# Kernel optimization log

Hardware: AMD Instinct MI355X
Metric: run time of the kernel (lower is better)

## Reference

```python
import jax, jax.numpy as jnp
import numpy as np

B, N, L = 64, 256, 1024
OUT = L // 2   # ChebConv out_channels = Seq_len / 2
ALPHA = 0.5    # DirGNNConv default alpha


def _glorot(key, shape):
    # PyG ChebConv lins use glorot init
    lim = float(np.sqrt(6.0 / (shape[0] + shape[1])))
    return jax.random.uniform(key, shape, minval=-lim, maxval=lim, dtype=jnp.float32)


def setup_inputs() -> dict:
    key = jax.random.key(0)
    ks = jax.random.split(key, 8)
    x = jax.random.normal(ks[0], (B, N, L), dtype=jnp.float32)
    # dense per-sample adjacency; only used via nonzero() in torch, never enters math (K=1)
    At = jax.random.randint(ks[1], (B, N, N), 0, 2, dtype=jnp.int32)
    W_in = _glorot(ks[2], (L, OUT))
    b_in = jnp.zeros((OUT,), dtype=jnp.float32)
    W_out = _glorot(ks[3], (L, OUT))
    b_out = jnp.zeros((OUT,), dtype=jnp.float32)
    # DirGNNConv root Linear (kaiming-ish uniform; exact init irrelevant for correctness baseline)
    lim = float(1.0 / np.sqrt(L))
    W_root = jax.random.uniform(ks[4], (L, OUT), minval=-lim, maxval=lim, dtype=jnp.float32)
    b_root = jax.random.uniform(ks[5], (OUT,), minval=-lim, maxval=lim, dtype=jnp.float32)
    return {"x": x, "At": At, "W_in": W_in, "b_in": b_in,
            "W_out": W_out, "b_out": b_out, "W_root": W_root, "b_root": b_root}


def reference(x, At, W_in, b_in, W_out, b_out, W_root, b_root):
    # so the batched edge_index built from At.nonzero() never influences the output.
    # DirGNNConv: alpha * conv_out(x) + (1-alpha) * conv_in(x) + root_lin(x).
    xf = x.reshape(B * N, L)                        # [B*N, L]
    y = (ALPHA * (xf @ W_out + b_out)
         + (1.0 - ALPHA) * (xf @ W_in + b_in)
         + (xf @ W_root + b_root))                  # [B*N, OUT]
    return y.reshape(B, N, OUT)
```

## Files before the change

kernel.cpp:

```cpp
#include <hip/hip_runtime.h>
#include <stdint.h>

static constexpr int Kdim  = 1024;
static constexpr int Ncols = 512;

typedef __attribute__((ext_vector_type(8))) short bf16x8;
typedef __attribute__((ext_vector_type(4))) float f32x4;

__device__ __forceinline__ unsigned short f2bf(float f) {
  unsigned u = __builtin_bit_cast(unsigned, f);
  u += 0x7FFFu + ((u >> 16) & 1u);
  return (unsigned short)(u >> 16);
}
__device__ __forceinline__ unsigned f2bf2(float lo, float hi) {
  unsigned ul = __builtin_bit_cast(unsigned, lo);
  unsigned uh = __builtin_bit_cast(unsigned, hi);
  ul += 0x7FFFu + ((ul >> 16) & 1u);
  uh += 0x7FFFu + ((uh >> 16) & 1u);
  return (ul >> 16) | (uh & 0xFFFF0000u);
}

__device__ __forceinline__ void gl2lds16(const void* g, void* l) {
  __builtin_amdgcn_global_load_lds(
      (const __attribute__((address_space(1))) void*)g,
      (__attribute__((address_space(3))) void*)l, 16, 0, 0);
}

__global__ __launch_bounds__(256) void combine_w(
    const float* __restrict__ Win, const float* __restrict__ Wout,
    const float* __restrict__ Wroot, unsigned short* __restrict__ Wt)
{
  __shared__ unsigned short lds[32 * 36];
  const int bid = blockIdx.x;
  const int tk0 = (bid & 31) * 32;
  const int tn0 = (bid >> 5) * 32;
  const int t = threadIdx.x;
  {
    const int k  = t >> 3;
    const int nq = (t & 7) * 4;
    const int gi = (tk0 + k) * Ncols + tn0 + nq;
    const float4 wi = *(const float4*)(Win + gi);
    const float4 wo = *(const float4*)(Wout + gi);
    const float4 wr = *(const float4*)(Wroot + gi);
    lds[(nq + 0) * 36 + k] = f2bf(0.5f * (wi.x + wo.x) + wr.x);
    lds[(nq + 1) * 36 + k] = f2bf(0.5f * (wi.y + wo.y) + wr.y);
    lds[(nq + 2) * 36 + k] = f2bf(0.5f * (wi.z + wo.z) + wr.z);
    lds[(nq + 3) * 36 + k] = f2bf(0.5f * (wi.w + wo.w) + wr.w);
  }
  __syncthreads();
  {
    const int n  = t >> 3;
    const int k8 = (t & 7) * 4;
    const ushort4 v = *(const ushort4*)&lds[n * 36 + k8];
    *(ushort4*)(Wt + (size_t)(tn0 + n) * Kdim + tk0 + k8) = v;
  }
}

__global__ __launch_bounds__(256, 2) void gemm_fused2(
    const float* __restrict__ X, const unsigned short* __restrict__ Wt,
    const float* __restrict__ b_in, const float* __restrict__ b_out,
    const float* __restrict__ b_root, float* __restrict__ Y)
{
  __shared__ __attribute__((aligned(16))) short As[2 * 4096];
  __shared__ __attribute__((aligned(16))) short Bs[2 * 4096];

  const int bid = blockIdx.x;
  const int m0 = (bid & 127) * 128;
  const int n0 = (bid >> 7) * 128;

  const int t    = threadIdx.x;
  const int lane = t & 63;
  const int w    = t >> 6;
  const int wm   = w >> 1;
  const int wn   = w & 1;
  const int quad = lane >> 4;
  const int lm   = lane & 15;

  const int sr = t >> 1;
  const int sh = t & 1;
  const float* xp = X + (size_t)(m0 + sr) * Kdim + sh * 16;
  const int sw  = (sr >> 1) & 3;
  const int aw0 = sr * 32 + (((2 * sh) ^ sw) * 8);
  const int aw1 = sr * 32 + (((2 * sh + 1) ^ sw) * 8);

  const int srb = lane >> 2;
  const int ss  = lane & 3;
  const int sc  = ss ^ ((srb >> 1) & 3);
  const unsigned short* gB = Wt + (size_t)(n0 + w * 32 + srb) * Kdim + sc * 8;
  const int rowK = 16 * Kdim;
  const int lb0 = w * 1024;
  const int lb1 = w * 1024 + 512;

  const int slot = quad ^ ((lm >> 1) & 3);
  const int aoff = (wm * 64 + lm) * 32 + slot * 8;
  const int boff = (wn * 64 + lm) * 32 + slot * 8;

  f32x4 acc[4][4] = {};

  gl2lds16(gB,        &Bs[lb0]);
  gl2lds16(gB + rowK, &Bs[lb1]);
  {
    const float4 a0 = *(const float4*)(xp + 0);
    const float4 a1 = *(const float4*)(xp + 4);
    const float4 a2 = *(const float4*)(xp + 8);
    const float4 a3 = *(const float4*)(xp + 12);
    uint4 p0, p1;
    p0.x = f2bf2(a0.x, a0.y); p0.y = f2bf2(a0.z, a0.w);
    p0.z = f2bf2(a1.x, a1.y); p0.w = f2bf2(a1.z, a1.w);
    p1.x = f2bf2(a2.x, a2.y); p1.y = f2bf2(a2.z, a2.w);
    p1.z = f2bf2(a3.x, a3.y); p1.w = f2bf2(a3.z, a3.w);
    *(uint4*)&As[aw0] = p0;
    *(uint4*)&As[aw1] = p1;
  }

  #pragma unroll 1
  for (int it = 0; it < 32; ++it) {
    const int p = (it & 1) * 4096;
    const int q = p ^ 4096;
    __syncthreads();

    const int nx = (it < 31 ? it + 1 : 31) * 32;
    gl2lds16(gB + nx,        &Bs[q + lb0]);
    gl2lds16(gB + nx + rowK, &Bs[q + lb1]);
    const float4 a0 = *(const float4*)(xp + nx + 0);
    const float4 a1 = *(const float4*)(xp + nx + 4);
    const float4 a2 = *(const float4*)(xp + nx + 8);
    const float4 a3 = *(const float4*)(xp + nx + 12);

    bf16x8 af[4], bfr[4];
    #pragma unroll
    for (int i = 0; i < 4; ++i) af[i]  = *(const bf16x8*)&As[p + aoff + i * 512];
    #pragma unroll
    for (int j = 0; j < 4; ++j) bfr[j] = *(const bf16x8*)&Bs[p + boff + j * 512];
    #pragma unroll
    for (int i = 0; i < 4; ++i)
      #pragma unroll
      for (int j = 0; j < 4; ++j)
        acc[i][j] = __builtin_amdgcn_mfma_f32_16x16x32_bf16(af[i], bfr[j], acc[i][j], 0, 0, 0);

    uint4 p0, p1;
    p0.x = f2bf2(a0.x, a0.y); p0.y = f2bf2(a0.z, a0.w);
    p0.z = f2bf2(a1.x, a1.y); p0.w = f2bf2(a1.z, a1.w);
    p1.x = f2bf2(a2.x, a2.y); p1.y = f2bf2(a2.z, a2.w);
    p1.z = f2bf2(a3.x, a3.y); p1.w = f2bf2(a3.z, a3.w);
    *(uint4*)&As[q + aw0] = p0;
    *(uint4*)&As[q + aw1] = p1;
  }

  #pragma unroll
  for (int j = 0; j < 4; ++j) {
    const int gc = n0 + wn * 64 + j * 16 + lm;
    const float bias = 0.5f * (b_in[gc] + b_out[gc]) + b_root[gc];
    #pragma unroll
    for (int i = 0; i < 4; ++i) {
      const int gr = m0 + wm * 64 + i * 16 + quad * 4;
      float* yp = Y + (size_t)gr * Ncols + gc;
      #pragma unroll
      for (int r = 0; r < 4; ++r)
        yp[(size_t)r * Ncols] = acc[i][j][r] + bias;
    }
  }
}

extern "C" void kernel_launch(void* const* d_in, const int* in_sizes, int n_in,
                              void* d_out, int out_size, void* d_ws, size_t ws_size,
                              hipStream_t stream)
{
  const float* x      = (const float*)d_in[0];
  const float* W_in   = (const float*)d_in[2];
  const float* b_in   = (const float*)d_in[3];
  const float* W_out  = (const float*)d_in[4];
  const float* b_out  = (const float*)d_in[5];
  const float* W_root = (const float*)d_in[6];
  const float* b_root = (const float*)d_in[7];
  float* y = (float*)d_out;

  unsigned short* Wt = (unsigned short*)d_ws;

  combine_w <<<dim3(512), dim3(256), 0, stream>>>(W_in, W_out, W_root, Wt);
  gemm_fused2<<<dim3(512), dim3(256), 0, stream>>>(x, Wt, b_in, b_out, b_root, y);
}
```

Baseline: 161.4 us.

## Load fp32 X tiles directly to LDS and convert to bf16 at fragment read

The GEMM now streams the fp32 activation tile into LDS with asynchronous global_load_lds instead of loading into registers, converting, and storing bf16. The bf16 conversion moves to the point where each MFMA fragment is read from LDS. The M tile shrinks from 128 to 64 rows, which doubles the grid to 1024 blocks and raises the occupancy hint to 4 blocks per CU. B uses a new XOR swizzle. The aim is to take the global-load latency and conversion off the critical path and raise concurrency. The costs are more LDS traffic for fp32 A, repeated conversion work per wave, and less reuse of B per block.

```diff
diff --git a/kernel.cpp b/kernel.cpp
--- a/kernel.cpp
+++ b/kernel.cpp
@@ -6,6 +6,8 @@
 
 typedef __attribute__((ext_vector_type(8))) short bf16x8;
 typedef __attribute__((ext_vector_type(4))) float f32x4;
+
+union pk8 { uint4 u; bf16x8 h; };
 
 __device__ __forceinline__ unsigned short f2bf(float f) {
   unsigned u = __builtin_bit_cast(unsigned, f);
@@ -56,17 +58,17 @@
   }
 }
 
-__global__ __launch_bounds__(256, 2) void gemm_fused2(
+__global__ __launch_bounds__(256, 4) void gemm_fused3(
     const float* __restrict__ X, const unsigned short* __restrict__ Wt,
     const float* __restrict__ b_in, const float* __restrict__ b_out,
     const float* __restrict__ b_root, float* __restrict__ Y)
 {
-  __shared__ __attribute__((aligned(16))) short As[2 * 4096];
-  __shared__ __attribute__((aligned(16))) short Bs[2 * 4096];
+  __shared__ __attribute__((aligned(16))) float As[2][64 * 32];
+  __shared__ __attribute__((aligned(16))) short Bs[2][128 * 32];
 
   const int bid = blockIdx.x;
-  const int m0 = (bid & 127) * 128;
-  const int n0 = (bid >> 7) * 128;
+  const int m0 = (bid & 255) * 64;
+  const int n0 = (bid >> 8) * 128;
 
   const int t    = threadIdx.x;
   const int lane = t & 63;
@@ -76,75 +78,70 @@
   const int quad = lane >> 4;
   const int lm   = lane & 15;
 
-  const int sr = t >> 1;
-  const int sh = t & 1;
-  const float* xp = X + (size_t)(m0 + sr) * Kdim + sh * 16;
-  const int sw  = (sr >> 1) & 3;
-  const int aw0 = sr * 32 + (((2 * sh) ^ sw) * 8);
-  const int aw1 = sr * 32 + (((2 * sh + 1) ^ sw) * 8);
+  const int ra = lane >> 3;
+  const int sa = lane & 7;
+  const int ca = sa ^ ra;
+  const float* gA0 = X + (size_t)(m0 + w * 16 + ra) * Kdim + ca * 4;
+  const float* gA1 = gA0 + (size_t)8 * Kdim;
+  const int lA0 = (w * 16) * 32;
+  const int lA1 = (w * 16 + 8) * 32;
 
-  const int srb = lane >> 2;
-  const int ss  = lane & 3;
-  const int sc  = ss ^ ((srb >> 1) & 3);
-  const unsigned short* gB = Wt + (size_t)(n0 + w * 32 + srb) * Kdim + sc * 8;
-  const int rowK = 16 * Kdim;
-  const int lb0 = w * 1024;
-  const int lb1 = w * 1024 + 512;
+  const int rb = lane >> 2;
+  const int sb = lane & 3;
+  const int cb = sb ^ ((rb ^ (rb >> 2)) & 3);
+  const unsigned short* gB0 = Wt + (size_t)(n0 + w * 32 + rb) * Kdim + cb * 8;
+  const unsigned short* gB1 = gB0 + (size_t)16 * Kdim;
+  const int lB0 = (w * 32) * 32;
+  const int lB1 = (w * 32 + 16) * 32;
 
-  const int slot = quad ^ ((lm >> 1) & 3);
-  const int aoff = (wm * 64 + lm) * 32 + slot * 8;
-  const int boff = (wn * 64 + lm) * 32 + slot * 8;
+  const int sA0 = (2 * quad) ^ (lm & 7);
+  const int sA1 = sA0 ^ 1;
+  const int aoff = (wm * 32 + lm) * 32;
+  const int swzB = quad ^ ((lm ^ (lm >> 2)) & 3);
+  const int boff = (wn * 64 + lm) * 32 + swzB * 8;
 
-  f32x4 acc[4][4] = {};
+  f32x4 acc[2][4] = {};
 
-  gl2lds16(gB,        &Bs[lb0]);
-  gl2lds16(gB + rowK, &Bs[lb1]);
-  {
-    const float4 a0 = *(const float4*)(xp + 0);
-    const float4 a1 = *(const float4*)(xp + 4);
-    const float4 a2 = *(const float4*)(xp + 8);
-    const float4 a3 = *(const float4*)(xp + 12);
-    uint4 p0, p1;
-    p0.x = f2bf2(a0.x, a0.y); p0.y = f2bf2(a0.z, a0.w);
-    p0.z = f2bf2(a1.x, a1.y); p0.w = f2bf2(a1.z, a1.w);
-    p1.x = f2bf2(a2.x, a2.y); p1.y = f2bf2(a2.z, a2.w);
-    p1.z = f2bf2(a3.x, a3.y); p1.w = f2bf2(a3.z, a3.w);
-    *(uint4*)&As[aw0] = p0;
-    *(uint4*)&As[aw1] = p1;
-  }
+  gl2lds16(gA0, &As[0][lA0]);
+  gl2lds16(gA1, &As[0][lA1]);
+  gl2lds16(gB0, &Bs[0][lB0]);
+  gl2lds16(gB1, &Bs[0][lB1]);
 
   #pragma unroll 1
   for (int it = 0; it < 32; ++it) {
-    const int p = (it & 1) * 4096;
-    const int q = p ^ 4096;
+    const int p = it & 1;
+    const int q = p ^ 1;
     __syncthreads();
 
     const int nx = (it < 31 ? it + 1 : 31) * 32;
-    gl2lds16(gB + nx,        &Bs[q + lb0]);
-    gl2lds16(gB + nx + rowK, &Bs[q + lb1]);
-    const float4 a0 = *(const float4*)(xp + nx + 0);
-    const float4 a1 = *(const float4*)(xp + nx + 4);
-    const float4 a2 = *(const float4*)(xp + nx + 8);
-    const float4 a3 = *(const float4*)(xp + nx + 12);
+    gl2lds16(gA0 + nx, &As[q][lA0]);
+    gl2lds16(gA1 + nx, &As[q][lA1]);
+    gl2lds16(gB0 + nx, &Bs[q][lB0]);
+    gl2lds16(gB1 + nx, &Bs[q][lB1]);
 
-    bf16x8 af[4], bfr[4];
+    bf16x8 bfr[4];
     #pragma unroll
-    for (int i = 0; i < 4; ++i) af[i]  = *(const bf16x8*)&As[p + aoff + i * 512];
+    for (int j = 0; j < 4; ++j)
+      bfr[j] = *(const bf16x8*)&Bs[p][boff + j * 512];
+
+    bf16x8 af[2];
     #pragma unroll
-    for (int j = 0; j < 4; ++j) bfr[j] = *(const bf16x8*)&Bs[p + boff + j * 512];
+    for (int i = 0; i < 2; ++i) {
+      const f32x4 lo = *(const f32x4*)&As[p][aoff + i * 512 + sA0 * 4];
+      const f32x4 hi = *(const f32x4*)&As[p][aoff + i * 512 + sA1 * 4];
+      pk8 pk;
+      pk.u.x = f2bf2(lo.x, lo.y);
+      pk.u.y = f2bf2(lo.z, lo.w);
+      pk.u.z = f2bf2(hi.x, hi.y);
+      pk.u.w = f2bf2(hi.z, hi.w);
+      af[i] = pk.h;
+    }
+
     #pragma unroll
-    for (int i = 0; i < 4; ++i)
+    for (int i = 0; i < 2; ++i)
       #pragma unroll
       for (int j = 0; j < 4; ++j)
         acc[i][j] = __builtin_amdgcn_mfma_f32_16x16x32_bf16(af[i], bfr[j], acc[i][j], 0, 0, 0);
-
-    uint4 p0, p1;
-    p0.x = f2bf2(a0.x, a0.y); p0.y = f2bf2(a0.z, a0.w);
-    p0.z = f2bf2(a1.x, a1.y); p0.w = f2bf2(a1.z, a1.w);
-    p1.x = f2bf2(a2.x, a2.y); p1.y = f2bf2(a2.z, a2.w);
-    p1.z = f2bf2(a3.x, a3.y); p1.w = f2bf2(a3.z, a3.w);
-    *(uint4*)&As[q + aw0] = p0;
-    *(uint4*)&As[q + aw1] = p1;
   }
 
   #pragma unroll
@@ -152,8 +149,8 @@
     const int gc = n0 + wn * 64 + j * 16 + lm;
     const float bias = 0.5f * (b_in[gc] + b_out[gc]) + b_root[gc];
     #pragma unroll
-    for (int i = 0; i < 4; ++i) {
-      const int gr = m0 + wm * 64 + i * 16 + quad * 4;
+    for (int i = 0; i < 2; ++i) {
+      const int gr = m0 + wm * 32 + i * 16 + quad * 4;
       float* yp = Y + (size_t)gr * Ncols + gc;
       #pragma unroll
       for (int r = 0; r < 4; ++r)
@@ -177,6 +174,6 @@
 
   unsigned short* Wt = (unsigned short*)d_ws;
 
-  combine_w <<<dim3(512), dim3(256), 0, stream>>>(W_in, W_out, W_root, Wt);
-  gemm_fused2<<<dim3(512), dim3(256), 0, stream>>>(x, Wt, b_in, b_out, b_root, y);
+  combine_w <<<dim3(512),  dim3(256), 0, stream>>>(W_in, W_out, W_root, Wt);
+  gemm_fused3<<<dim3(1024), dim3(256), 0, stream>>>(x, Wt, b_in, b_out, b_root, y);
 }
```

Result: no change. 160.3 us (-0.7%).
